# Performance work log

Hardware: AMD Instinct MI355X
Metric: run time of the kernel (lower is better)

The kernel has to match this reference:

```python
import jax, jax.numpy as jnp
import numpy as np

N, E, S, D, T, H = 100000, 1600000, 16, 32, 16, 64
LN_EPS = 1e-5


def setup_inputs():
    key = jax.random.key(0)
    ks = jax.random.split(key, 12)
    p = lambda k, shp, s=0.05: jax.random.normal(k, shp, dtype=jnp.float32) * s
    return {
        'x': jax.random.normal(ks[0], (N, S + D, T), dtype=jnp.float32),
        'graph': jax.random.randint(ks[1], (2, E), 0, N, dtype=jnp.int32),
        'gru_Wih': p(ks[2], (3 * H, D)),
        'gru_Whh': p(ks[3], (3 * H, H)),
        'gru_bih': jnp.zeros((3 * H,), jnp.float32),
        'gru_bhh': jnp.zeros((3 * H,), jnp.float32),
        'gc_W1': p(ks[4], (S, 32)),
        'gc_b1': jnp.zeros((32,), jnp.float32),
        'gc_W2': p(ks[5], (32, 64)),
        'gc_b2': jnp.zeros((64,), jnp.float32),
        'ln_g': jnp.ones((H + 64,), jnp.float32),
        'ln_b': jnp.zeros((H + 64,), jnp.float32),
        'lin1_W': p(ks[6], (H + 64, 64)),
        'lin1_b': jnp.zeros((64,), jnp.float32),
        'lin2_W': p(ks[7], (64, 64)),
        'lin2_b': jnp.zeros((64,), jnp.float32),
        'out_W': p(ks[8], (64, 1)),
        'out_b': jnp.zeros((1,), jnp.float32),
    }


def _gru_last(x_temporal, Wih, Whh, bih, bhh):
    # x_temporal: [B, T, D] -> last hidden state [B, H] (torch GRU gate order r,z,n)
    xp = jnp.einsum('btd,gd->btg', x_temporal, Wih) + bih  # [B, T, 3H]
    xp = jnp.transpose(xp, (1, 0, 2))  # [T, B, 3H]

    def step(h, xt):
        gh = h @ Whh.T + bhh
        xr, xz, xn = jnp.split(xt, 3, axis=-1)
        hr, hz, hn = jnp.split(gh, 3, axis=-1)
        r = jax.nn.sigmoid(xr + hr)
        z = jax.nn.sigmoid(xz + hz)
        n = jnp.tanh(xn + r * hn)
        h = (1.0 - z) * n + z * h
        return h, None

    h0 = jnp.zeros((x_temporal.shape[0], H), x_temporal.dtype)
    h_last, _ = jax.lax.scan(step, h0, xp)
    return h_last


def _graph_conv(h, src, dst, norm_src, norm_dst, W, b):
    # DGL GraphConv with norm='both': D_out^{-1/2} A D_in^{-1/2} h W + b
    h = h * norm_src[:, None]
    m = jax.ops.segment_sum(h[src], dst, num_segments=N)
    m = m * norm_dst[:, None]
    return m @ W + b


def reference(x, graph, gru_Wih, gru_Whh, gru_bih, gru_bhh, gc_W1, gc_b1,
              gc_W2, gc_b2, ln_g, ln_b, lin1_W, lin1_b, lin2_W, lin2_b,
              out_W, out_b):
    # --- temporal branch: GRU over temporal features, keep last step ---
    x_temporal = jnp.transpose(x[:, S:, :], (0, 2, 1))  # [B, T, D]
    lstm_out = _gru_last(x_temporal, gru_Wih, gru_Whh, gru_bih, gru_bhh)

    src, dst = graph[0], graph[1]
    ones_e = jnp.ones((E,), x.dtype)
    deg_out = jax.ops.segment_sum(ones_e, src, num_segments=N)
    deg_in = jax.ops.segment_sum(ones_e, dst, num_segments=N)
    norm_src = jnp.maximum(deg_out, 1.0) ** -0.5
    norm_dst = jnp.maximum(deg_in, 1.0) ** -0.5

    h = x[:, :S, 0]  # [B, S] static features at t=0
    h = jax.nn.relu(_graph_conv(h, src, dst, norm_src, norm_dst, gc_W1, gc_b1))
    h = jax.nn.relu(_graph_conv(h, src, dst, norm_src, norm_dst, gc_W2, gc_b2))

    # --- fusion head (dropout is identity in eval) ---
    z = jnp.concatenate([lstm_out, h], axis=1)  # [B, 128]
    mu = jnp.mean(z, axis=-1, keepdims=True)
    var = jnp.mean((z - mu) ** 2, axis=-1, keepdims=True)
    z = (z - mu) * jax.lax.rsqrt(var + LN_EPS) * ln_g + ln_b
    z = jax.nn.relu(z @ lin1_W + lin1_b)
    hidden = jax.nn.relu(z @ lin2_W + lin2_b)
    logits = hidden @ out_W + out_b
    output = logits
    return (output, logits, hidden)
```

## Files before the change

### kernel.cpp

```cpp
#include <hip/hip_runtime.h>
#include <hip/hip_bf16.h>
#include <stdint.h>

#define NN 100000
#define EE 1600000
#define RS 4096
#define NRANGE 25
#define NCH 32
#define CHSZ (EE/NCH)

#define SC_RZ (-1.44269504f)
#define SC_N  (2.88539008f)

typedef float f32x4 __attribute__((ext_vector_type(4)));
typedef short bf16x8 __attribute__((ext_vector_type(8)));

#define MFMA(A,B,C) __builtin_amdgcn_mfma_f32_16x16x32_bf16((A),(B),(C),0,0,0)

__device__ __forceinline__ unsigned short f2bf(float f) {
  union { float f; unsigned u; } v; v.f = f;
  unsigned r = v.u + 0x7fffu + ((v.u >> 16) & 1u);
  return (unsigned short)(r >> 16);
}
__device__ __forceinline__ float bflo(unsigned u) {
  union { unsigned u; float f; } v; v.u = u << 16; return v.f;
}
__device__ __forceinline__ float bfhi(unsigned u) {
  union { unsigned u; float f; } v; v.u = u & 0xffff0000u; return v.f;
}

__device__ __forceinline__ unsigned pk2(float lo, float hi) {
  __hip_bfloat162 t = __float22bfloat162_rn(make_float2(lo, hi));
  unsigned r;
  __builtin_memcpy(&r, &t, 4);
  return r;
}
__device__ __forceinline__ bf16x8 packbf(f32x4 a, f32x4 b) {
  union { unsigned u[4]; bf16x8 v; } r;
  r.u[0] = pk2(a[0], a[1]);
  r.u[1] = pk2(a[2], a[3]);
  r.u[2] = pk2(b[0], b[1]);
  r.u[3] = pk2(b[2], b[3]);
  return r.v;
}

__device__ __forceinline__ float exp2fast(float x) {
#if __has_builtin(__builtin_amdgcn_exp2f)
  return __builtin_amdgcn_exp2f(x);
#else
  return exp2f(x);
#endif
}

__global__ __launch_bounds__(256) void k_init(const float* __restrict__ Wih, const float* __restrict__ Whh,
                                              const float* __restrict__ bih, const float* __restrict__ bhh,
                                              const float* __restrict__ W1, const float* __restrict__ W2,
                                              unsigned short* __restrict__ wihA, unsigned short* __restrict__ whhA,
                                              unsigned short* __restrict__ w1A, unsigned short* __restrict__ w2A,
                                              float* __restrict__ bsum) {
  int idx = blockIdx.x * 256 + threadIdx.x;
  if (idx < 6144) {
    int e = idx & 7, l = (idx >> 3) & 63, mt = idx >> 9;
    int p = l & 15, q = l >> 4;
    float s = (mt < 8) ? SC_RZ : SC_N;
    wihA[idx] = f2bf(Wih[(mt * 16 + p) * 32 + 8 * q + e] * s);
    return;
  }
  idx -= 6144;
  if (idx < 12288) {
    int e = idx & 7, l = (idx >> 3) & 63, fid = idx >> 9;
    int mt = fid >> 1, kt = fid & 1, p = l & 15, q = l >> 4;
    int j = kt * 32 + 16 * (e >> 2) + 4 * q + (e & 3);
    float s = (mt < 8) ? SC_RZ : SC_N;
    whhA[idx] = f2bf(Whh[(mt * 16 + p) * 64 + j] * s);
    return;
  }
  idx -= 12288;
  if (idx < 8192) {
    int e = idx & 7, l = (idx >> 3) & 63, fid = idx >> 9;
    int mt = fid >> 2, kt = fid & 3, p = l & 15, q = l >> 4;
    w1A[idx] = f2bf(W1[(kt * 32 + 8 * q + e) * 64 + mt * 16 + p]);
    return;
  }
  idx -= 8192;
  if (idx < 4096) {
    int e = idx & 7, l = (idx >> 3) & 63, fid = idx >> 9;
    int mt = fid >> 1, kt = fid & 1, p = l & 15, q = l >> 4;
    int k = kt * 32 + 16 * (e >> 2) + 4 * q + (e & 3);
    w2A[idx] = f2bf(W2[k * 64 + mt * 16 + p]);
    return;
  }
  idx -= 4096;
  if (idx < 192) {
    float s = (idx < 128) ? SC_RZ : SC_N;
    bsum[idx] = (bih[idx] + bhh[idx]) * s;
  }
}

__global__ __launch_bounds__(256) void k_count(const int* __restrict__ graph,
                                               unsigned short* __restrict__ cntS,
                                               unsigned short* __restrict__ cntD) {
  __shared__ unsigned hS[RS];
  __shared__ unsigned hD[RS];
  int tid = threadIdx.x;
  int c = blockIdx.x & (NCH - 1), r = blockIdx.x >> 5;
  int r0 = r * RS;
  for (int j = tid; j < RS; j += 256) { hS[j] = 0; hD[j] = 0; }
  __syncthreads();
  const int4* sv = (const int4*)(graph + c * CHSZ);
  const int4* dv = (const int4*)(graph + EE + c * CHSZ);
  for (int i = tid; i < CHSZ / 4; i += 256) {
    int4 s4 = sv[i];
    int4 d4 = dv[i];
    int ss[4] = {s4.x, s4.y, s4.z, s4.w};
    int dd[4] = {d4.x, d4.y, d4.z, d4.w};
#pragma unroll
    for (int k = 0; k < 4; ++k) {
      unsigned us = (unsigned)(ss[k] - r0);
      if (us < RS) atomicAdd(&hS[us], 1u);
      unsigned ud = (unsigned)(dd[k] - r0);
      if (ud < RS) atomicAdd(&hD[ud], 1u);
    }
  }
  __syncthreads();
  for (int j = tid; j < RS; j += 256) {
    int n = r0 + j;
    if (n < NN) {
      cntS[(size_t)c * NN + n] = (unsigned short)hS[j];
      cntD[(size_t)c * NN + n] = (unsigned short)hD[j];
    }
  }
}

__global__ __launch_bounds__(256) void k_reduce(const unsigned short* __restrict__ cntS,
                                                const unsigned short* __restrict__ cntD,
                                                unsigned* __restrict__ degO,
                                                unsigned* __restrict__ degI) {
  int n = blockIdx.x * 256 + threadIdx.x;
  if (n >= NN) return;
  unsigned a = 0, b = 0;
#pragma unroll
  for (int c = 0; c < NCH; ++c) {
    a += cntS[(size_t)c * NN + n];
    b += cntD[(size_t)c * NN + n];
  }
  degO[n] = a;
  degI[n] = b;
}

__global__ __launch_bounds__(256) void k_scan1(const unsigned* __restrict__ degI,
                                               unsigned* __restrict__ offs,
                                               unsigned* __restrict__ bsums) {
  __shared__ unsigned sd[256];
  int tid = threadIdx.x;
  int base = blockIdx.x * 1024 + tid * 4;
  unsigned v0 = base + 0 < NN ? degI[base + 0] : 0;
  unsigned v1 = base + 1 < NN ? degI[base + 1] : 0;
  unsigned v2 = base + 2 < NN ? degI[base + 2] : 0;
  unsigned v3 = base + 3 < NN ? degI[base + 3] : 0;
  unsigned ts = v0 + v1 + v2 + v3;
  sd[tid] = ts;
  __syncthreads();
  for (int o = 1; o < 256; o <<= 1) {
    unsigned xv = (tid >= o) ? sd[tid - o] : 0;
    __syncthreads();
    sd[tid] += xv;
    __syncthreads();
  }
  unsigned run = sd[tid] - ts;
  if (base + 0 < NN) offs[base + 0] = run; run += v0;
  if (base + 1 < NN) offs[base + 1] = run; run += v1;
  if (base + 2 < NN) offs[base + 2] = run; run += v2;
  if (base + 3 < NN) offs[base + 3] = run;
  if (tid == 255) bsums[blockIdx.x] = sd[255];
}

__global__ __launch_bounds__(256) void k_scan23(unsigned* __restrict__ offs,
                                                const unsigned* __restrict__ bsums,
                                                const unsigned short* __restrict__ cntD,
                                                unsigned* __restrict__ curstart,
                                                float* __restrict__ h0s,
                                                const unsigned* __restrict__ degO) {
  __shared__ unsigned sb[128];
  int tid = threadIdx.x;
  if (tid < 128) sb[tid] = (tid < 98) ? bsums[tid] : 0;
  __syncthreads();
  for (int o = 1; o < 128; o <<= 1) {
    unsigned xv = (tid < 128 && tid >= o) ? sb[tid - o] : 0;
    __syncthreads();
    if (tid < 128) sb[tid] += xv;
    __syncthreads();
  }
  int n = blockIdx.x * 256 + tid;
  if (n < NN) {
    int b = n >> 10;
    unsigned add = b ? sb[b - 1] : 0;
    unsigned v = offs[n] + add;
    offs[n] = v;
    unsigned run = v;
#pragma unroll
    for (int c = 0; c < NCH; ++c) {
      curstart[(size_t)c * NN + n] = run;
      run += cntD[(size_t)c * NN + n];
    }
    float sc = rsqrtf(fmaxf((float)degO[n], 1.0f));
    f32x4* hp = (f32x4*)(h0s + (size_t)n * 16);
#pragma unroll
    for (int i = 0; i < 4; ++i) {
      f32x4 hv = hp[i];
#pragma unroll
      for (int e = 0; e < 4; ++e) hv[e] *= sc;
      hp[i] = hv;
    }
  }
  if (n == 0) offs[NN] = EE;
}

__global__ __launch_bounds__(256) void k_fill(const int* __restrict__ graph,
                                              const unsigned* __restrict__ curstart,
                                              unsigned* __restrict__ eidx) {
  __shared__ unsigned cur[RS];
  int tid = threadIdx.x;
  int c = blockIdx.x & (NCH - 1), r = blockIdx.x >> 5;
  int r0 = r * RS;
  for (int j = tid; j < RS; j += 256) {
    int n = r0 + j;
    cur[j] = (n < NN) ? curstart[(size_t)c * NN + n] : 0u;
  }
  __syncthreads();
  const int4* sv = (const int4*)(graph + c * CHSZ);
  const int4* dv = (const int4*)(graph + EE + c * CHSZ);
  for (int i = tid; i < CHSZ / 4; i += 256) {
    int4 s4 = sv[i];
    int4 d4 = dv[i];
    int ss[4] = {s4.x, s4.y, s4.z, s4.w};
    int dd[4] = {d4.x, d4.y, d4.z, d4.w};
#pragma unroll
    for (int k = 0; k < 4; ++k) {
      unsigned ud = (unsigned)(dd[k] - r0);
      if (ud < RS) {
        unsigned pos = atomicAdd(&cur[ud], 1u);
        eidx[pos] = (unsigned)ss[k];
      }
    }
  }
}

__global__ __launch_bounds__(256) void k_transpose(const float* __restrict__ x,
                                                   unsigned short* __restrict__ xT,
                                                   float* __restrict__ h0) {
  __shared__ float st[8 * 816];
  int tid = threadIdx.x;
  size_t n0 = (size_t)blockIdx.x * 8;
  const float* xb = x + n0 * 768;
#pragma unroll
  for (int i = 0; i < 6; ++i) {
    int w0 = i * 1024 + tid * 4;
    int n = ((w0 >> 8) * 0xAAAB) >> 17;
    int r = w0 - n * 768;
    f32x4 v = *(const f32x4*)(xb + w0);
    float* dp = st + n * 816 + (r >> 4) * 17 + (r & 15);
    dp[0] = v[0]; dp[1] = v[1]; dp[2] = v[2]; dp[3] = v[3];
  }
  __syncthreads();
  if (tid < 128) {
    int hn = tid >> 4, hs = tid & 15;
    h0[(n0 + hn) * 16 + hs] = st[hn * 816 + hs * 17];
  }
#pragma unroll
  for (int j = 0; j < 2; ++j) {
    int o = j * 256 + tid;
    int n = o >> 6, idx = o & 63, t = idx >> 2, k8 = idx & 3;
    const float* sp = st + n * 816 + (16 + 8 * k8) * 17 + t;
    unsigned a0 = f2bf(sp[0])  | ((unsigned)f2bf(sp[17])  << 16);
    unsigned a1 = f2bf(sp[34]) | ((unsigned)f2bf(sp[51])  << 16);
    unsigned a2 = f2bf(sp[68]) | ((unsigned)f2bf(sp[85])  << 16);
    unsigned a3 = f2bf(sp[102])| ((unsigned)f2bf(sp[119]) << 16);
    ((uint4*)xT)[n0 * 64 + o] = uint4{a0, a1, a2, a3};
  }
}

__global__ __launch_bounds__(256) void k_conv1(const unsigned* __restrict__ offs,
                                               const unsigned* __restrict__ eidx,
                                               const float* __restrict__ h0s,
                                               const unsigned* __restrict__ degI,
                                               const unsigned* __restrict__ degO,
                                               const float* __restrict__ W1,
                                               const float* __restrict__ b1,
                                               unsigned short* __restrict__ h1s) {
  __shared__ float sW[512];
  __shared__ float sb[32];
  __shared__ float sm[4][16];
  int tid = threadIdx.x;
  sW[tid] = W1[tid]; sW[256 + tid] = W1[256 + tid];
  if (tid < 32) sb[tid] = b1[tid];
  int wave = tid >> 6, lane = tid & 63;
  int n = blockIdx.x * 4 + wave;
  int slot = lane >> 4, f = lane & 15;
  unsigned k0 = offs[n], k1 = offs[n + 1];
  float acc = 0.0f;
  for (unsigned k = k0 + slot; k < k1; k += 4)
    acc += h0s[(size_t)eidx[k] * 16 + f];
  acc += __shfl_xor(acc, 16);
  acc += __shfl_xor(acc, 32);
  acc *= rsqrtf(fmaxf((float)degI[n], 1.0f));
  if (slot == 0) sm[wave][f] = acc;
  __syncthreads();
  if (lane < 32) {
    float o = sb[lane];
#pragma unroll
    for (int i = 0; i < 16; ++i) o += sm[wave][i] * sW[i * 32 + lane];
    float sc = rsqrtf(fmaxf((float)degO[n], 1.0f));
    h1s[(size_t)n * 32 + lane] = f2bf(fmaxf(o, 0.0f) * sc);
  }
}

__global__ __launch_bounds__(256) void k_conv2(const unsigned* __restrict__ offs,
                                               const unsigned* __restrict__ eidx,
                                               const unsigned* __restrict__ h1u,
                                               const unsigned* __restrict__ degI,
                                               const float* __restrict__ W2,
                                               const float* __restrict__ b2,
                                               unsigned short* __restrict__ hgnn) {
  __shared__ float sW[2048];
  __shared__ float sb[64];
  __shared__ float sm[4][32];
  int tid = threadIdx.x;
  for (int i = tid; i < 2048; i += 256) sW[i] = W2[i];
  if (tid < 64) sb[tid] = b2[tid];
  int wave = tid >> 6, lane = tid & 63;
  int n = blockIdx.x * 4 + wave;
  int slot = lane >> 4, fu = lane & 15;
  unsigned k0 = offs[n], k1 = offs[n + 1];
  float a0 = 0.0f, a1 = 0.0f;
  for (unsigned k = k0 + slot; k < k1; k += 4) {
    unsigned u = h1u[(size_t)eidx[k] * 16 + fu];
    a0 += bflo(u); a1 += bfhi(u);
  }
  a0 += __shfl_xor(a0, 16); a0 += __shfl_xor(a0, 32);
  a1 += __shfl_xor(a1, 16); a1 += __shfl_xor(a1, 32);
  float sc = rsqrtf(fmaxf((float)degI[n], 1.0f));
  if (slot == 0) { sm[wave][2 * fu] = a0 * sc; sm[wave][2 * fu + 1] = a1 * sc; }
  __syncthreads();
  float o = sb[lane];
#pragma unroll
  for (int i = 0; i < 32; ++i) o += sm[wave][i] * sW[i * 64 + lane];
  hgnn[(size_t)n * 64 + lane] = f2bf(fmaxf(o, 0.0f));
}

__global__ __launch_bounds__(256, 2) void k_gru(const unsigned short* __restrict__ xT,
                                                const unsigned short* __restrict__ wihA,
                                                const unsigned short* __restrict__ whhA,
                                                const float* __restrict__ bsum,
                                                const float* __restrict__ bih,
                                                const float* __restrict__ bhh,
                                                unsigned* __restrict__ lstm) {
  __shared__ __align__(16) unsigned short sWih[6144];
  __shared__ __align__(16) float sB[576];
  int tid = threadIdx.x;
  for (int i = tid; i < 768; i += 256) ((uint4*)sWih)[i] = ((const uint4*)wihA)[i];
  if (tid < 192) {
    float scn = (tid >= 128) ? SC_N : 1.0f;
    sB[tid] = bsum[tid];
    sB[192 + tid] = bih[tid] * scn;
    sB[384 + tid] = bhh[tid] * scn;
  }
  __syncthreads();
  int wave = tid >> 6, lane = tid & 63;
  int gw = blockIdx.x * 4 + wave;
  int nb = gw * 32;
  if (nb >= NN) return;
  int p = lane & 15, q = lane >> 4;
  const unsigned short* xw0 = xT + (size_t)(nb + p) * 512 + q * 8;
  const unsigned short* xw1 = xT + (size_t)(nb + 16 + p) * 512 + q * 8;
  const bf16x8* wv = (const bf16x8*)sWih;
  const bf16x8* gh = (const bf16x8*)whhA;
  bf16x8 whhR[24];
#pragma unroll
  for (int fid = 0; fid < 24; ++fid) whhR[fid] = gh[fid * 64 + lane];
  f32x4 hT[2][4] = {};
  bf16x8 hb[2][2] = {};
  uint4 xl0 = *(const uint4*)xw0;
  uint4 xl1 = *(const uint4*)xw1;
#pragma unroll 1
  for (int t = 0; t < 16; ++t) {
    asm volatile("" ::: "memory");
    bf16x8 xb0 = __builtin_bit_cast(bf16x8, xl0);
    bf16x8 xb1 = __builtin_bit_cast(bf16x8, xl1);
    if (t < 15) {
      xl0 = *(const uint4*)(xw0 + (t + 1) * 32);
      xl1 = *(const uint4*)(xw1 + (t + 1) * 32);
    }
#pragma unroll
    for (int i = 0; i < 4; ++i) {
      f32x4 br = *(const f32x4*)(sB + i * 16 + 4 * q);
      f32x4 bz = *(const f32x4*)(sB + 64 + i * 16 + 4 * q);
      f32x4 bn = *(const f32x4*)(sB + 320 + i * 16 + 4 * q);
      f32x4 bh = *(const f32x4*)(sB + 512 + i * 16 + 4 * q);
      f32x4 ar0 = br, ar1 = br, az0 = bz, az1 = bz, an0 = bn, an1 = bn, ah0 = bh, ah1 = bh;
      bf16x8 w;
      w = wv[i * 64 + lane];        ar0 = MFMA(w, xb0, ar0); ar1 = MFMA(w, xb1, ar1);
      w = wv[(4 + i) * 64 + lane];  az0 = MFMA(w, xb0, az0); az1 = MFMA(w, xb1, az1);
      w = wv[(8 + i) * 64 + lane];  an0 = MFMA(w, xb0, an0); an1 = MFMA(w, xb1, an1);
#pragma unroll
      for (int kt = 0; kt < 2; ++kt) {
        ar0 = MFMA(whhR[i * 2 + kt], hb[0][kt], ar0);
        ar1 = MFMA(whhR[i * 2 + kt], hb[1][kt], ar1);
        az0 = MFMA(whhR[8 + i * 2 + kt], hb[0][kt], az0);
        az1 = MFMA(whhR[8 + i * 2 + kt], hb[1][kt], az1);
        ah0 = MFMA(whhR[16 + i * 2 + kt], hb[0][kt], ah0);
        ah1 = MFMA(whhR[16 + i * 2 + kt], hb[1][kt], ah1);
      }
#pragma unroll
      for (int e = 0; e < 4; ++e) {
        float r0 = __builtin_amdgcn_rcpf(1.0f + exp2fast(ar0[e]));
        float z0 = __builtin_amdgcn_rcpf(1.0f + exp2fast(az0[e]));
        float n0 = 1.0f - 2.0f * __builtin_amdgcn_rcpf(exp2fast(an0[e] + r0 * ah0[e]) + 1.0f);
        hT[0][i][e] = n0 + z0 * (hT[0][i][e] - n0);
        float r1 = __builtin_amdgcn_rcpf(1.0f + exp2fast(ar1[e]));
        float z1 = __builtin_amdgcn_rcpf(1.0f + exp2fast(az1[e]));
        float n1 = 1.0f - 2.0f * __builtin_amdgcn_rcpf(exp2fast(an1[e] + r1 * ah1[e]) + 1.0f);
        hT[1][i][e] = n1 + z1 * (hT[1][i][e] - n1);
      }
    }
    hb[0][0] = packbf(hT[0][0], hT[0][1]); hb[0][1] = packbf(hT[0][2], hT[0][3]);
    hb[1][0] = packbf(hT[1][0], hT[1][1]); hb[1][1] = packbf(hT[1][2], hT[1][3]);
  }
  unsigned* lw0 = lstm + (size_t)(nb + p) * 32 + 2 * q;
  unsigned* lw1 = lstm + (size_t)(nb + 16 + p) * 32 + 2 * q;
#pragma unroll
  for (int i = 0; i < 4; ++i) {
    lw0[i * 8]     = pk2(hT[0][i][0], hT[0][i][1]);
    lw0[i * 8 + 1] = pk2(hT[0][i][2], hT[0][i][3]);
    lw1[i * 8]     = pk2(hT[1][i][0], hT[1][i][1]);
    lw1[i * 8 + 1] = pk2(hT[1][i][2], hT[1][i][3]);
  }
}

__global__ __launch_bounds__(256) void k_final(const unsigned short* __restrict__ lstm,
                                               const unsigned short* __restrict__ hgnn,
                                               const unsigned short* __restrict__ w1A,
                                               const unsigned short* __restrict__ w2A,
                                               const float* __restrict__ b1,
                                               const float* __restrict__ b2,
                                               const float* __restrict__ lng,
                                               const float* __restrict__ lnb,
                                               const float* __restrict__ outw,
                                               const float* __restrict__ outb,
                                               float* __restrict__ out) {
  __shared__ __align__(16) unsigned short sW1[8192];
  __shared__ __align__(16) unsigned short sW2[4096];
  __shared__ __align__(16) float sP[452];
  int tid = threadIdx.x;
  for (int i = tid; i < 1024; i += 256) ((uint4*)sW1)[i] = ((const uint4*)w1A)[i];
  for (int i = tid; i < 512; i += 256)  ((uint4*)sW2)[i] = ((const uint4*)w2A)[i];
  if (tid < 64) sP[tid] = b1[tid];
  if (tid >= 64 && tid < 128) sP[tid] = b2[tid - 64];
  if (tid < 128) { sP[128 + tid] = lng[tid]; sP[256 + tid] = lnb[tid]; }
  if (tid < 64) sP[384 + tid] = outw[tid];
  if (tid == 0) sP[448] = outb[0];
  __syncthreads();
  int wave = tid >> 6, lane = tid & 63;
  int gw = blockIdx.x * 4 + wave;
  int nb = gw * 16;
  if (nb >= NN) return;
  int s = lane & 15, q = lane >> 4;
  const unsigned short* Ls = lstm + (size_t)(nb + s) * 64;
  const unsigned short* Gs = hgnn + (size_t)(nb + s) * 64;
  float zv[4][8];
#pragma unroll
  for (int blk = 0; blk < 2; ++blk) {
    uint4 lv = *(const uint4*)(Ls + blk * 32 + 8 * q);
    uint4 gv = *(const uint4*)(Gs + blk * 32 + 8 * q);
    unsigned lu[4] = {lv.x, lv.y, lv.z, lv.w};
    unsigned gu[4] = {gv.x, gv.y, gv.z, gv.w};
#pragma unroll
    for (int k = 0; k < 4; ++k) {
      zv[blk][2 * k] = bflo(lu[k]);     zv[blk][2 * k + 1] = bfhi(lu[k]);
      zv[2 + blk][2 * k] = bflo(gu[k]); zv[2 + blk][2 * k + 1] = bfhi(gu[k]);
    }
  }
  float sum = 0.0f, ss = 0.0f;
#pragma unroll
  for (int blk = 0; blk < 4; ++blk)
#pragma unroll
    for (int e = 0; e < 8; ++e) { float v = zv[blk][e]; sum += v; ss += v * v; }
  sum += __shfl_xor(sum, 16); sum += __shfl_xor(sum, 32);
  ss += __shfl_xor(ss, 16);  ss += __shfl_xor(ss, 32);
  float mu = sum * (1.0f / 128.0f);
  float var = ss * (1.0f / 128.0f) - mu * mu;
  float inv = rsqrtf(var + 1e-5f);
  bf16x8 zb[4];
#pragma unroll
  for (int blk = 0; blk < 4; ++blk) {
    bf16x8 r;
#pragma unroll
    for (int e = 0; e < 8; ++e) {
      int f = blk * 32 + 8 * q + e;
      float zn = (zv[blk][e] - mu) * inv * sP[128 + f] + sP[256 + f];
      r[e] = (short)f2bf(zn);
    }
    zb[blk] = r;
  }
  const bf16x8* w1v = (const bf16x8*)sW1;
  const bf16x8* w2v = (const bf16x8*)sW2;
  f32x4 c1[4];
#pragma unroll
  for (int mt = 0; mt < 4; ++mt) {
    c1[mt] = *(const f32x4*)(sP + mt * 16 + 4 * q);
#pragma unroll
    for (int kt = 0; kt < 4; ++kt)
      c1[mt] = MFMA(w1v[(mt * 4 + kt) * 64 + lane], zb[kt], c1[mt]);
#pragma unroll
    for (int e = 0; e < 4; ++e) c1[mt][e] = fmaxf(c1[mt][e], 0.0f);
  }
  bf16x8 h1b[2] = { packbf(c1[0], c1[1]), packbf(c1[2], c1[3]) };
  f32x4 c2[4];
  float partial = 0.0f;
  float* hid = out + 2 * (size_t)NN + (size_t)(nb + s) * 64;
#pragma unroll
  for (int mt = 0; mt < 4; ++mt) {
    c2[mt] = *(const f32x4*)(sP + 64 + mt * 16 + 4 * q);
#pragma unroll
    for (int kt = 0; kt < 2; ++kt)
      c2[mt] = MFMA(w2v[(mt * 2 + kt) * 64 + lane], h1b[kt], c2[mt]);
#pragma unroll
    for (int e = 0; e < 4; ++e) c2[mt][e] = fmaxf(c2[mt][e], 0.0f);
    *(f32x4*)(hid + mt * 16 + 4 * q) = c2[mt];
    f32x4 ow = *(const f32x4*)(sP + 384 + mt * 16 + 4 * q);
#pragma unroll
    for (int e = 0; e < 4; ++e) partial += c2[mt][e] * ow[e];
  }
  partial += __shfl_xor(partial, 16);
  partial += __shfl_xor(partial, 32);
  if (q == 0) {
    float lg = partial + sP[448];
    out[nb + s] = lg;
    out[(size_t)NN + nb + s] = lg;
  }
}

extern "C" void kernel_launch(void* const* d_in, const int* in_sizes, int n_in,
                              void* d_out, int out_size, void* d_ws, size_t ws_size,
                              hipStream_t stream) {
  const float* x   = (const float*)d_in[0];
  const int* graph = (const int*)d_in[1];
  const float* Wih = (const float*)d_in[2];
  const float* Whh = (const float*)d_in[3];
  const float* bih = (const float*)d_in[4];
  const float* bhh = (const float*)d_in[5];
  const float* W1  = (const float*)d_in[6];
  const float* b1  = (const float*)d_in[7];
  const float* W2  = (const float*)d_in[8];
  const float* b2  = (const float*)d_in[9];
  const float* lng = (const float*)d_in[10];
  const float* lnb = (const float*)d_in[11];
  const float* l1W = (const float*)d_in[12];
  const float* l1b = (const float*)d_in[13];
  const float* l2W = (const float*)d_in[14];
  const float* l2b = (const float*)d_in[15];
  const float* oW  = (const float*)d_in[16];
  const float* ob  = (const float*)d_in[17];
  float* out = (float*)d_out;

  char* w = (char*)d_ws;
  unsigned short* xT  = (unsigned short*)(w + 0);
  float* h0s          = (float*)(w + 102400000);
  unsigned* degO      = (unsigned*)(w + 108800000);
  unsigned* degI      = (unsigned*)(w + 109200000);
  unsigned* offs      = (unsigned*)(w + 109600000);
  unsigned* bsums     = (unsigned*)(w + 110400256);
  unsigned* eidx      = (unsigned*)(w + 110400768);
  unsigned short* h1s = (unsigned short*)(w + 116800768);
  unsigned short* hgnn= (unsigned short*)(w + 129600768);
  unsigned* lstm      = (unsigned*)(w + 155200768);
  unsigned short* wihA= (unsigned short*)(w + 180800768);
  unsigned short* whhA= (unsigned short*)(w + 180813056);
  unsigned short* w1A = (unsigned short*)(w + 180837632);
  unsigned short* w2A = (unsigned short*)(w + 180854016);
  float* bsum         = (float*)(w + 180862208);
  if (ws_size < 180862976u) return;
  unsigned short* cntD16 = (unsigned short*)(w + 116800768);
  unsigned short* cntS16 = (unsigned short*)(w + 155200768);
  unsigned* curstart     = (unsigned*)(w + 129600768);

  k_init<<<121, 256, 0, stream>>>(Wih, Whh, bih, bhh, l1W, l2W, wihA, whhA, w1A, w2A, bsum);
  k_transpose<<<12500, 256, 0, stream>>>(x, xT, h0s);
  k_count<<<NRANGE * NCH, 256, 0, stream>>>(graph, cntS16, cntD16);
  k_reduce<<<391, 256, 0, stream>>>(cntS16, cntD16, degO, degI);
  k_scan1<<<98, 256, 0, stream>>>(degI, offs, bsums);
  k_scan23<<<391, 256, 0, stream>>>(offs, bsums, cntD16, curstart, h0s, degO);
  k_fill<<<NRANGE * NCH, 256, 0, stream>>>(graph, curstart, eidx);
  k_conv1<<<25000, 256, 0, stream>>>(offs, eidx, h0s, degI, degO, W1, b1, h1s);
  k_conv2<<<25000, 256, 0, stream>>>(offs, eidx, (const unsigned*)h1s, degI, W2, b2, hgnn);
  k_gru<<<782, 256, 0, stream>>>(xT, wihA, whhA, bsum, bih, bhh, lstm);
  k_final<<<1563, 256, 0, stream>>>((const unsigned short*)lstm, hgnn,
                                    w1A, w2A, l1b, l2b, lng, lnb, oW, ob, out);
}
```

Baseline: 444.6 us.

## Merge independent preprocessing kernels into combined launches to overlap work

Fuses the weight-init, x-transpose and degree-count kernels into one launch that dispatches on block index, and folds the degree reduction into the scan kernels. The GRU recurrence and the CSR fill now share a single launch, so the compute-bound GRU blocks can run alongside the atomic-heavy fill blocks. This cuts launch count and tail gaps between dependent stages. In exchange, both merged kernels must use the larger shared-memory footprint and the GRU's register budget, which may reduce occupancy for the lighter block types.

New measurement: 431.9 us, median of 2. 2.9% less time.

```diff
diff --git a/kernel.cpp b/kernel.cpp
--- a/kernel.cpp
+++ b/kernel.cpp
@@ -52,13 +52,86 @@
 #endif
 }
 
-__global__ __launch_bounds__(256) void k_init(const float* __restrict__ Wih, const float* __restrict__ Whh,
-                                              const float* __restrict__ bih, const float* __restrict__ bhh,
-                                              const float* __restrict__ W1, const float* __restrict__ W2,
-                                              unsigned short* __restrict__ wihA, unsigned short* __restrict__ whhA,
-                                              unsigned short* __restrict__ w1A, unsigned short* __restrict__ w2A,
-                                              float* __restrict__ bsum) {
-  int idx = blockIdx.x * 256 + threadIdx.x;
+__global__ __launch_bounds__(256) void k_front(const float* __restrict__ x,
+                                               unsigned short* __restrict__ xT,
+                                               float* __restrict__ h0,
+                                               const int* __restrict__ graph,
+                                               unsigned short* __restrict__ cntS,
+                                               unsigned short* __restrict__ cntD,
+                                               const float* __restrict__ Wih, const float* __restrict__ Whh,
+                                               const float* __restrict__ bih, const float* __restrict__ bhh,
+                                               const float* __restrict__ W1, const float* __restrict__ W2,
+                                               unsigned short* __restrict__ wihA, unsigned short* __restrict__ whhA,
+                                               unsigned short* __restrict__ w1A, unsigned short* __restrict__ w2A,
+                                               float* __restrict__ bsum) {
+  __shared__ __align__(16) char smem[32768];
+  int tid = threadIdx.x;
+  unsigned b = blockIdx.x;
+  if (b < 12500) {
+    float* st = (float*)smem;
+    size_t n0 = (size_t)b * 8;
+    const float* xb = x + n0 * 768;
+#pragma unroll
+    for (int i = 0; i < 6; ++i) {
+      int w0 = i * 1024 + tid * 4;
+      int n = ((w0 >> 8) * 0xAAAB) >> 17;
+      int r = w0 - n * 768;
+      f32x4 v = *(const f32x4*)(xb + w0);
+      float* dp = st + n * 816 + (r >> 4) * 17 + (r & 15);
+      dp[0] = v[0]; dp[1] = v[1]; dp[2] = v[2]; dp[3] = v[3];
+    }
+    __syncthreads();
+    if (tid < 128) {
+      int hn = tid >> 4, hs = tid & 15;
+      h0[(n0 + hn) * 16 + hs] = st[hn * 816 + hs * 17];
+    }
+#pragma unroll
+    for (int j = 0; j < 2; ++j) {
+      int o = j * 256 + tid;
+      int n = o >> 6, idx = o & 63, t = idx >> 2, k8 = idx & 3;
+      const float* sp = st + n * 816 + (16 + 8 * k8) * 17 + t;
+      unsigned a0 = f2bf(sp[0])  | ((unsigned)f2bf(sp[17])  << 16);
+      unsigned a1 = f2bf(sp[34]) | ((unsigned)f2bf(sp[51])  << 16);
+      unsigned a2 = f2bf(sp[68]) | ((unsigned)f2bf(sp[85])  << 16);
+      unsigned a3 = f2bf(sp[102])| ((unsigned)f2bf(sp[119]) << 16);
+      ((uint4*)xT)[n0 * 64 + o] = uint4{a0, a1, a2, a3};
+    }
+    return;
+  }
+  if (b < 13300) {
+    unsigned* hS = (unsigned*)smem;
+    unsigned* hD = (unsigned*)(smem + 16384);
+    int cb = b - 12500;
+    int c = cb & (NCH - 1), r = cb >> 5;
+    int r0 = r * RS;
+    for (int j = tid; j < RS; j += 256) { hS[j] = 0; hD[j] = 0; }
+    __syncthreads();
+    const int4* sv = (const int4*)(graph + c * CHSZ);
+    const int4* dv = (const int4*)(graph + EE + c * CHSZ);
+    for (int i = tid; i < CHSZ / 4; i += 256) {
+      int4 s4 = sv[i];
+      int4 d4 = dv[i];
+      int ss[4] = {s4.x, s4.y, s4.z, s4.w};
+      int dd[4] = {d4.x, d4.y, d4.z, d4.w};
+#pragma unroll
+      for (int k = 0; k < 4; ++k) {
+        unsigned us = (unsigned)(ss[k] - r0);
+        if (us < RS) atomicAdd(&hS[us], 1u);
+        unsigned ud = (unsigned)(dd[k] - r0);
+        if (ud < RS) atomicAdd(&hD[ud], 1u);
+      }
+    }
+    __syncthreads();
+    for (int j = tid; j < RS; j += 256) {
+      int n = r0 + j;
+      if (n < NN) {
+        cntS[(size_t)c * NN + n] = (unsigned short)hS[j];
+        cntD[(size_t)c * NN + n] = (unsigned short)hD[j];
+      }
+    }
+    return;
+  }
+  int idx = (b - 13300) * 256 + tid;
   if (idx < 6144) {
     int e = idx & 7, l = (idx >> 3) & 63, mt = idx >> 9;
     int p = l & 15, q = l >> 4;
@@ -97,68 +170,35 @@
   }
 }
 
-__global__ __launch_bounds__(256) void k_count(const int* __restrict__ graph,
-                                               unsigned short* __restrict__ cntS,
-                                               unsigned short* __restrict__ cntD) {
-  __shared__ unsigned hS[RS];
-  __shared__ unsigned hD[RS];
-  int tid = threadIdx.x;
-  int c = blockIdx.x & (NCH - 1), r = blockIdx.x >> 5;
-  int r0 = r * RS;
-  for (int j = tid; j < RS; j += 256) { hS[j] = 0; hD[j] = 0; }
-  __syncthreads();
-  const int4* sv = (const int4*)(graph + c * CHSZ);
-  const int4* dv = (const int4*)(graph + EE + c * CHSZ);
-  for (int i = tid; i < CHSZ / 4; i += 256) {
-    int4 s4 = sv[i];
-    int4 d4 = dv[i];
-    int ss[4] = {s4.x, s4.y, s4.z, s4.w};
-    int dd[4] = {d4.x, d4.y, d4.z, d4.w};
-#pragma unroll
-    for (int k = 0; k < 4; ++k) {
-      unsigned us = (unsigned)(ss[k] - r0);
-      if (us < RS) atomicAdd(&hS[us], 1u);
-      unsigned ud = (unsigned)(dd[k] - r0);
-      if (ud < RS) atomicAdd(&hD[ud], 1u);
-    }
-  }
-  __syncthreads();
-  for (int j = tid; j < RS; j += 256) {
-    int n = r0 + j;
-    if (n < NN) {
-      cntS[(size_t)c * NN + n] = (unsigned short)hS[j];
-      cntD[(size_t)c * NN + n] = (unsigned short)hD[j];
-    }
-  }
-}
-
-__global__ __launch_bounds__(256) void k_reduce(const unsigned short* __restrict__ cntS,
-                                                const unsigned short* __restrict__ cntD,
-                                                unsigned* __restrict__ degO,
-                                                unsigned* __restrict__ degI) {
-  int n = blockIdx.x * 256 + threadIdx.x;
-  if (n >= NN) return;
-  unsigned a = 0, b = 0;
-#pragma unroll
-  for (int c = 0; c < NCH; ++c) {
-    a += cntS[(size_t)c * NN + n];
-    b += cntD[(size_t)c * NN + n];
-  }
-  degO[n] = a;
-  degI[n] = b;
-}
-
-__global__ __launch_bounds__(256) void k_scan1(const unsigned* __restrict__ degI,
+__global__ __launch_bounds__(256) void k_scan1(const unsigned short* __restrict__ cntD,
+                                               unsigned* __restrict__ degI,
                                                unsigned* __restrict__ offs,
                                                unsigned* __restrict__ bsums) {
   __shared__ unsigned sd[256];
   int tid = threadIdx.x;
   int base = blockIdx.x * 1024 + tid * 4;
-  unsigned v0 = base + 0 < NN ? degI[base + 0] : 0;
-  unsigned v1 = base + 1 < NN ? degI[base + 1] : 0;
-  unsigned v2 = base + 2 < NN ? degI[base + 2] : 0;
-  unsigned v3 = base + 3 < NN ? degI[base + 3] : 0;
-  unsigned ts = v0 + v1 + v2 + v3;
+  unsigned s0 = 0, s1 = 0, s2 = 0, s3 = 0;
+  if (base + 3 < NN) {
+#pragma unroll
+    for (int c = 0; c < NCH; ++c) {
+      uint2 u = *(const uint2*)(cntD + (size_t)c * NN + base);
+      s0 += u.x & 0xffffu; s1 += u.x >> 16;
+      s2 += u.y & 0xffffu; s3 += u.y >> 16;
+    }
+  } else {
+#pragma unroll
+    for (int c = 0; c < NCH; ++c) {
+      if (base + 0 < NN) s0 += cntD[(size_t)c * NN + base + 0];
+      if (base + 1 < NN) s1 += cntD[(size_t)c * NN + base + 1];
+      if (base + 2 < NN) s2 += cntD[(size_t)c * NN + base + 2];
+      if (base + 3 < NN) s3 += cntD[(size_t)c * NN + base + 3];
+    }
+  }
+  if (base + 0 < NN) degI[base + 0] = s0;
+  if (base + 1 < NN) degI[base + 1] = s1;
+  if (base + 2 < NN) degI[base + 2] = s2;
+  if (base + 3 < NN) degI[base + 3] = s3;
+  unsigned ts = s0 + s1 + s2 + s3;
   sd[tid] = ts;
   __syncthreads();
   for (int o = 1; o < 256; o <<= 1) {
@@ -168,9 +208,9 @@
     __syncthreads();
   }
   unsigned run = sd[tid] - ts;
-  if (base + 0 < NN) offs[base + 0] = run; run += v0;
-  if (base + 1 < NN) offs[base + 1] = run; run += v1;
-  if (base + 2 < NN) offs[base + 2] = run; run += v2;
+  if (base + 0 < NN) offs[base + 0] = run; run += s0;
+  if (base + 1 < NN) offs[base + 1] = run; run += s1;
+  if (base + 2 < NN) offs[base + 2] = run; run += s2;
   if (base + 3 < NN) offs[base + 3] = run;
   if (tid == 255) bsums[blockIdx.x] = sd[255];
 }
@@ -178,9 +218,10 @@
 __global__ __launch_bounds__(256) void k_scan23(unsigned* __restrict__ offs,
                                                 const unsigned* __restrict__ bsums,
                                                 const unsigned short* __restrict__ cntD,
+                                                const unsigned short* __restrict__ cntS,
                                                 unsigned* __restrict__ curstart,
-                                                float* __restrict__ h0s,
-                                                const unsigned* __restrict__ degO) {
+                                                unsigned* __restrict__ degO,
+                                                float* __restrict__ h0s) {
   __shared__ unsigned sb[128];
   int tid = threadIdx.x;
   if (tid < 128) sb[tid] = (tid < 98) ? bsums[tid] : 0;
@@ -198,12 +239,15 @@
     unsigned v = offs[n] + add;
     offs[n] = v;
     unsigned run = v;
+    unsigned a = 0;
 #pragma unroll
     for (int c = 0; c < NCH; ++c) {
       curstart[(size_t)c * NN + n] = run;
       run += cntD[(size_t)c * NN + n];
-    }
-    float sc = rsqrtf(fmaxf((float)degO[n], 1.0f));
+      a += cntS[(size_t)c * NN + n];
+    }
+    degO[n] = a;
+    float sc = rsqrtf(fmaxf((float)a, 1.0f));
     f32x4* hp = (f32x4*)(h0s + (size_t)n * 16);
 #pragma unroll
     for (int i = 0; i < 4; ++i) {
@@ -216,67 +260,124 @@
   if (n == 0) offs[NN] = EE;
 }
 
-__global__ __launch_bounds__(256) void k_fill(const int* __restrict__ graph,
-                                              const unsigned* __restrict__ curstart,
-                                              unsigned* __restrict__ eidx) {
-  __shared__ unsigned cur[RS];
+__global__ __launch_bounds__(256, 2) void k_gf(const unsigned short* __restrict__ xT,
+                                               const unsigned short* __restrict__ wihA,
+                                               const unsigned short* __restrict__ whhA,
+                                               const float* __restrict__ bsum,
+                                               const float* __restrict__ bih,
+                                               const float* __restrict__ bhh,
+                                               unsigned* __restrict__ lstm,
+                                               const int* __restrict__ graph,
+                                               const unsigned* __restrict__ curstart,
+                                               unsigned* __restrict__ eidx) {
+  __shared__ __align__(16) char smem[16640];
   int tid = threadIdx.x;
-  int c = blockIdx.x & (NCH - 1), r = blockIdx.x >> 5;
-  int r0 = r * RS;
-  for (int j = tid; j < RS; j += 256) {
-    int n = r0 + j;
-    cur[j] = (n < NN) ? curstart[(size_t)c * NN + n] : 0u;
+  if (blockIdx.x >= 782) {
+    unsigned* cur = (unsigned*)smem;
+    int cb = blockIdx.x - 782;
+    int c = cb & (NCH - 1), r = cb >> 5;
+    int r0 = r * RS;
+    for (int j = tid; j < RS; j += 256) {
+      int n = r0 + j;
+      cur[j] = (n < NN) ? curstart[(size_t)c * NN + n] : 0u;
+    }
+    __syncthreads();
+    const int4* sv = (const int4*)(graph + c * CHSZ);
+    const int4* dv = (const int4*)(graph + EE + c * CHSZ);
+    for (int i = tid; i < CHSZ / 4; i += 256) {
+      int4 s4 = sv[i];
+      int4 d4 = dv[i];
+      int ss[4] = {s4.x, s4.y, s4.z, s4.w};
+      int dd[4] = {d4.x, d4.y, d4.z, d4.w};
+#pragma unroll
+      for (int k = 0; k < 4; ++k) {
+        unsigned ud = (unsigned)(dd[k] - r0);
+        if (ud < RS) {
+          unsigned pos = atomicAdd(&cur[ud], 1u);
+          eidx[pos] = (unsigned)ss[k];
+        }
+      }
+    }
+    return;
+  }
+  unsigned short* sWih = (unsigned short*)smem;
+  float* sB = (float*)(smem + 12288);
+  for (int i = tid; i < 768; i += 256) ((uint4*)sWih)[i] = ((const uint4*)wihA)[i];
+  if (tid < 192) {
+    float scn = (tid >= 128) ? SC_N : 1.0f;
+    sB[tid] = bsum[tid];
+    sB[192 + tid] = bih[tid] * scn;
+    sB[384 + tid] = bhh[tid] * scn;
   }
   __syncthreads();
-  const int4* sv = (const int4*)(graph + c * CHSZ);
-  const int4* dv = (const int4*)(graph + EE + c * CHSZ);
-  for (int i = tid; i < CHSZ / 4; i += 256) {
-    int4 s4 = sv[i];
-    int4 d4 = dv[i];
-    int ss[4] = {s4.x, s4.y, s4.z, s4.w};
-    int dd[4] = {d4.x, d4.y, d4.z, d4.w};
-#pragma unroll
-    for (int k = 0; k < 4; ++k) {
-      unsigned ud = (unsigned)(dd[k] - r0);
-      if (ud < RS) {
-        unsigned pos = atomicAdd(&cur[ud], 1u);
-        eidx[pos] = (unsigned)ss[k];
+  int wave = tid >> 6, lane = tid & 63;
+  int gw = blockIdx.x * 4 + wave;
+  int nb = gw * 32;
+  if (nb >= NN) return;
+  int p = lane & 15, q = lane >> 4;
+  const unsigned short* xw0 = xT + (size_t)(nb + p) * 512 + q * 8;
+  const unsigned short* xw1 = xT + (size_t)(nb + 16 + p) * 512 + q * 8;
+  const bf16x8* wv = (const bf16x8*)sWih;
+  const bf16x8* gh = (const bf16x8*)whhA;
+  bf16x8 whhR[24];
+#pragma unroll
+  for (int fid = 0; fid < 24; ++fid) whhR[fid] = gh[fid * 64 + lane];
+  f32x4 hT[2][4] = {};
+  bf16x8 hb[2][2] = {};
+  uint4 xl0 = *(const uint4*)xw0;
+  uint4 xl1 = *(const uint4*)xw1;
+#pragma unroll 1
+  for (int t = 0; t < 16; ++t) {
+    asm volatile("" ::: "memory");
+    bf16x8 xb0 = __builtin_bit_cast(bf16x8, xl0);
+    bf16x8 xb1 = __builtin_bit_cast(bf16x8, xl1);
+    if (t < 15) {
+      xl0 = *(const uint4*)(xw0 + (t + 1) * 32);
+      xl1 = *(const uint4*)(xw1 + (t + 1) * 32);
+    }
+#pragma unroll
+    for (int i = 0; i < 4; ++i) {
+      f32x4 br = *(const f32x4*)(sB + i * 16 + 4 * q);
+      f32x4 bz = *(const f32x4*)(sB + 64 + i * 16 + 4 * q);
+      f32x4 bn = *(const f32x4*)(sB + 320 + i * 16 + 4 * q);
+      f32x4 bh = *(const f32x4*)(sB + 512 + i * 16 + 4 * q);
+      f32x4 ar0 = br, ar1 = br, az0 = bz, az1 = bz, an0 = bn, an1 = bn, ah0 = bh, ah1 = bh;
+      bf16x8 w;
+      w = wv[i * 64 + lane];        ar0 = MFMA(w, xb0, ar0); ar1 = MFMA(w, xb1, ar1);
+      w = wv[(4 + i) * 64 + lane];  az0 = MFMA(w, xb0, az0); az1 = MFMA(w, xb1, az1);
+      w = wv[(8 + i) * 64 + lane];  an0 = MFMA(w, xb0, an0); an1 = MFMA(w, xb1, an1);
+#pragma unroll
+      for (int kt = 0; kt < 2; ++kt) {
+        ar0 = MFMA(whhR[i * 2 + kt], hb[0][kt], ar0);
+        ar1 = MFMA(whhR[i * 2 + kt], hb[1][kt], ar1);
+        az0 = MFMA(whhR[8 + i * 2 + kt], hb[0][kt], az0);
+        az1 = MFMA(whhR[8 + i * 2 + kt], hb[1][kt], az1);
+        ah0 = MFMA(whhR[16 + i * 2 + kt], hb[0][kt], ah0);
+        ah1 = MFMA(whhR[16 + i * 2 + kt], hb[1][kt], ah1);
       }
-    }
-  }
-}
-
-__global__ __launch_bounds__(256) void k_transpose(const float* __restrict__ x,
-                                                   unsigned short* __restrict__ xT,
-                                                   float* __restrict__ h0) {
-  __shared__ float st[8 * 816];
-  int tid = threadIdx.x;
-  size_t n0 = (size_t)blockIdx.x * 8;
-  const float* xb = x + n0 * 768;
-#pragma unroll
-  for (int i = 0; i < 6; ++i) {
-    int w0 = i * 1024 + tid * 4;
-    int n = ((w0 >> 8) * 0xAAAB) >> 17;
-    int r = w0 - n * 768;
-    f32x4 v = *(const f32x4*)(xb + w0);
-    float* dp = st + n * 816 + (r >> 4) * 17 + (r & 15);
-    dp[0] = v[0]; dp[1] = v[1]; dp[2] = v[2]; dp[3] = v[3];
-  }
-  __syncthreads();
-  if (tid < 128) {
-    int hn = tid >> 4, hs = tid & 15;
-    h0[(n0 + hn) * 16 + hs] = st[hn * 816 + hs * 17];
-  }
-#pragma unroll
-  for (int j = 0; j < 2; ++j) {
-    int o = j * 256 + tid;
-    int n = o >> 6, idx = o & 63, t = idx >> 2, k8 = idx & 3;
-    const float* sp = st + n * 816 + (16 + 8 * k8) * 17 + t;
-    unsigned a0 = f2bf(sp[0])  | ((unsigned)f2bf(sp[17])  << 16);
-    unsigned a1 = f2bf(sp[34]) | ((unsigned)f2bf(sp[51])  << 16);
-    unsigned a2 = f2bf(sp[68]) | ((unsigned)f2bf(sp[85])  << 16);
-    unsigned a3 = f2bf(sp[102])| ((unsigned)f2bf(sp[119]) << 16);
-    ((uint4*)xT)[n0 * 64 + o] = uint4{a0, a1, a2, a3};
+#pragma unroll
+      for (int e = 0; e < 4; ++e) {
+        float r0 = __builtin_amdgcn_rcpf(1.0f + exp2fast(ar0[e]));
+        float z0 = __builtin_amdgcn_rcpf(1.0f + exp2fast(az0[e]));
+        float n0 = 1.0f - 2.0f * __builtin_amdgcn_rcpf(exp2fast(an0[e] + r0 * ah0[e]) + 1.0f);
+        hT[0][i][e] = n0 + z0 * (hT[0][i][e] - n0);
+        float r1 = __builtin_amdgcn_rcpf(1.0f + exp2fast(ar1[e]));
+        float z1 = __builtin_amdgcn_rcpf(1.0f + exp2fast(az1[e]));
+        float n1 = 1.0f - 2.0f * __builtin_amdgcn_rcpf(exp2fast(an1[e] + r1 * ah1[e]) + 1.0f);
+        hT[1][i][e] = n1 + z1 * (hT[1][i][e] - n1);
+      }
+    }
+    hb[0][0] = packbf(hT[0][0], hT[0][1]); hb[0][1] = packbf(hT[0][2], hT[0][3]);
+    hb[1][0] = packbf(hT[1][0], hT[1][1]); hb[1][1] = packbf(hT[1][2], hT[1][3]);
+  }
+  unsigned* lw0 = lstm + (size_t)(nb + p) * 32 + 2 * q;
+  unsigned* lw1 = lstm + (size_t)(nb + 16 + p) * 32 + 2 * q;
+#pragma unroll
+  for (int i = 0; i < 4; ++i) {
+    lw0[i * 8]     = pk2(hT[0][i][0], hT[0][i][1]);
+    lw0[i * 8 + 1] = pk2(hT[0][i][2], hT[0][i][3]);
+    lw1[i * 8]     = pk2(hT[1][i][0], hT[1][i][1]);
+    lw1[i * 8 + 1] = pk2(hT[1][i][2], hT[1][i][3]);
   }
 }
 
@@ -346,95 +447,6 @@
 #pragma unroll
   for (int i = 0; i < 32; ++i) o += sm[wave][i] * sW[i * 64 + lane];
   hgnn[(size_t)n * 64 + lane] = f2bf(fmaxf(o, 0.0f));
-}
-
-__global__ __launch_bounds__(256, 2) void k_gru(const unsigned short* __restrict__ xT,
-                                                const unsigned short* __restrict__ wihA,
-                                                const unsigned short* __restrict__ whhA,
-                                                const float* __restrict__ bsum,
-                                                const float* __restrict__ bih,
-                                                const float* __restrict__ bhh,
-                                                unsigned* __restrict__ lstm) {
-  __shared__ __align__(16) unsigned short sWih[6144];
-  __shared__ __align__(16) float sB[576];
-  int tid = threadIdx.x;
-  for (int i = tid; i < 768; i += 256) ((uint4*)sWih)[i] = ((const uint4*)wihA)[i];
-  if (tid < 192) {
-    float scn = (tid >= 128) ? SC_N : 1.0f;
-    sB[tid] = bsum[tid];
-    sB[192 + tid] = bih[tid] * scn;
-    sB[384 + tid] = bhh[tid] * scn;
-  }
-  __syncthreads();
-  int wave = tid >> 6, lane = tid & 63;
-  int gw = blockIdx.x * 4 + wave;
-  int nb = gw * 32;
-  if (nb >= NN) return;
-  int p = lane & 15, q = lane >> 4;
-  const unsigned short* xw0 = xT + (size_t)(nb + p) * 512 + q * 8;
-  const unsigned short* xw1 = xT + (size_t)(nb + 16 + p) * 512 + q * 8;
-  const bf16x8* wv = (const bf16x8*)sWih;
-  const bf16x8* gh = (const bf16x8*)whhA;
-  bf16x8 whhR[24];
-#pragma unroll
-  for (int fid = 0; fid < 24; ++fid) whhR[fid] = gh[fid * 64 + lane];
-  f32x4 hT[2][4] = {};
-  bf16x8 hb[2][2] = {};
-  uint4 xl0 = *(const uint4*)xw0;
-  uint4 xl1 = *(const uint4*)xw1;
-#pragma unroll 1
-  for (int t = 0; t < 16; ++t) {
-    asm volatile("" ::: "memory");
-    bf16x8 xb0 = __builtin_bit_cast(bf16x8, xl0);
-    bf16x8 xb1 = __builtin_bit_cast(bf16x8, xl1);
-    if (t < 15) {
-      xl0 = *(const uint4*)(xw0 + (t + 1) * 32);
-      xl1 = *(const uint4*)(xw1 + (t + 1) * 32);
-    }
-#pragma unroll
-    for (int i = 0; i < 4; ++i) {
-      f32x4 br = *(const f32x4*)(sB + i * 16 + 4 * q);
-      f32x4 bz = *(const f32x4*)(sB + 64 + i * 16 + 4 * q);
-      f32x4 bn = *(const f32x4*)(sB + 320 + i * 16 + 4 * q);
-      f32x4 bh = *(const f32x4*)(sB + 512 + i * 16 + 4 * q);
-      f32x4 ar0 = br, ar1 = br, az0 = bz, az1 = bz, an0 = bn, an1 = bn, ah0 = bh, ah1 = bh;
-      bf16x8 w;
-      w = wv[i * 64 + lane];        ar0 = MFMA(w, xb0, ar0); ar1 = MFMA(w, xb1, ar1);
-      w = wv[(4 + i) * 64 + lane];  az0 = MFMA(w, xb0, az0); az1 = MFMA(w, xb1, az1);
-      w = wv[(8 + i) * 64 + lane];  an0 = MFMA(w, xb0, an0); an1 = MFMA(w, xb1, an1);
-#pragma unroll
-      for (int kt = 0; kt < 2; ++kt) {
-        ar0 = MFMA(whhR[i * 2 + kt], hb[0][kt], ar0);
-        ar1 = MFMA(whhR[i * 2 + kt], hb[1][kt], ar1);
-        az0 = MFMA(whhR[8 + i * 2 + kt], hb[0][kt], az0);
-        az1 = MFMA(whhR[8 + i * 2 + kt], hb[1][kt], az1);
-        ah0 = MFMA(whhR[16 + i * 2 + kt], hb[0][kt], ah0);
-        ah1 = MFMA(whhR[16 + i * 2 + kt], hb[1][kt], ah1);
-      }
-#pragma unroll
-      for (int e = 0; e < 4; ++e) {
-        float r0 = __builtin_amdgcn_rcpf(1.0f + exp2fast(ar0[e]));
-        float z0 = __builtin_amdgcn_rcpf(1.0f + exp2fast(az0[e]));
-        float n0 = 1.0f - 2.0f * __builtin_amdgcn_rcpf(exp2fast(an0[e] + r0 * ah0[e]) + 1.0f);
-        hT[0][i][e] = n0 + z0 * (hT[0][i][e] - n0);
-        float r1 = __builtin_amdgcn_rcpf(1.0f + exp2fast(ar1[e]));
-        float z1 = __builtin_amdgcn_rcpf(1.0f + exp2fast(az1[e]));
-        float n1 = 1.0f - 2.0f * __builtin_amdgcn_rcpf(exp2fast(an1[e] + r1 * ah1[e]) + 1.0f);
-        hT[1][i][e] = n1 + z1 * (hT[1][i][e] - n1);
-      }
-    }
-    hb[0][0] = packbf(hT[0][0], hT[0][1]); hb[0][1] = packbf(hT[0][2], hT[0][3]);
-    hb[1][0] = packbf(hT[1][0], hT[1][1]); hb[1][1] = packbf(hT[1][2], hT[1][3]);
-  }
-  unsigned* lw0 = lstm + (size_t)(nb + p) * 32 + 2 * q;
-  unsigned* lw1 = lstm + (size_t)(nb + 16 + p) * 32 + 2 * q;
-#pragma unroll
-  for (int i = 0; i < 4; ++i) {
-    lw0[i * 8]     = pk2(hT[0][i][0], hT[0][i][1]);
-    lw0[i * 8 + 1] = pk2(hT[0][i][2], hT[0][i][3]);
-    lw1[i * 8]     = pk2(hT[1][i][0], hT[1][i][1]);
-    lw1[i * 8 + 1] = pk2(hT[1][i][2], hT[1][i][3]);
-  }
 }
 
 __global__ __launch_bounds__(256) void k_final(const unsigned short* __restrict__ lstm,
@@ -584,16 +596,13 @@
   unsigned short* cntS16 = (unsigned short*)(w + 155200768);
   unsigned* curstart     = (unsigned*)(w + 129600768);
 
-  k_init<<<121, 256, 0, stream>>>(Wih, Whh, bih, bhh, l1W, l2W, wihA, whhA, w1A, w2A, bsum);
-  k_transpose<<<12500, 256, 0, stream>>>(x, xT, h0s);
-  k_count<<<NRANGE * NCH, 256, 0, stream>>>(graph, cntS16, cntD16);
-  k_reduce<<<391, 256, 0, stream>>>(cntS16, cntD16, degO, degI);
-  k_scan1<<<98, 256, 0, stream>>>(degI, offs, bsums);
-  k_scan23<<<391, 256, 0, stream>>>(offs, bsums, cntD16, curstart, h0s, degO);
-  k_fill<<<NRANGE * NCH, 256, 0, stream>>>(graph, curstart, eidx);
+  k_front<<<13421, 256, 0, stream>>>(x, xT, h0s, graph, cntS16, cntD16,
+                                     Wih, Whh, bih, bhh, l1W, l2W, wihA, whhA, w1A, w2A, bsum);
+  k_scan1<<<98, 256, 0, stream>>>(cntD16, degI, offs, bsums);
+  k_scan23<<<391, 256, 0, stream>>>(offs, bsums, cntD16, cntS16, curstart, degO, h0s);
+  k_gf<<<1582, 256, 0, stream>>>(xT, wihA, whhA, bsum, bih, bhh, lstm, graph, curstart, eidx);
   k_conv1<<<25000, 256, 0, stream>>>(offs, eidx, h0s, degI, degO, W1, b1, h1s);
   k_conv2<<<25000, 256, 0, stream>>>(offs, eidx, (const unsigned*)h1s, degI, W2, b2, hgnn);
-  k_gru<<<782, 256, 0, stream>>>(xT, wihA, whhA, bsum, bih, bhh, lstm);
   k_final<<<1563, 256, 0, stream>>>((const unsigned short*)lstm, hgnn,
                                     w1A, w2A, l1b, l2b, lng, lnb, oW, ob, out);
 }
```
